# Performance work log

Measured on AMD Instinct MI355X. Metric: run time of the kernel, lower is better.

## Reference

```python
import jax, jax.numpy as jnp
import numpy as np

N, B, L, D = 11, 4, 2048, 1024
EPS = 1e-5


def _layernorm(x, g, b):
    # torch LayerNorm: biased variance over last dim
    mu = x.mean(-1, keepdims=True)
    var = x.var(-1, keepdims=True)
    return (x - mu) / jnp.sqrt(var + EPS) * g + b


def _block_attn_res(V, q, g, b):
    # V: [n, B, L, D] -- completed blocks + current partial
    K = _layernorm(V, g, b)
    logits = jnp.einsum('d,nbld->nbl', q, K)      # single pseudo-query dot
    w = jax.nn.softmax(logits, axis=0)             # softmax over block dim n
    return jnp.einsum('nbl,nbld->bld', w, V)       # weighted sum back to [B,L,D]


def setup_inputs() -> dict:
    key = jax.random.key(0)
    k0, k1, k2 = jax.random.split(key, 3)
    return {
        'streams': jax.random.normal(k0, (N, B, L, D), dtype=jnp.float32),
        'attn_q': jax.random.normal(k1, (N, D), dtype=jnp.float32) * 0.02,
        'attn_gamma': jnp.ones((N, D), dtype=jnp.float32),
        'attn_beta': jnp.zeros((N, D), dtype=jnp.float32),
        'mlp_q': jax.random.normal(k2, (N, D), dtype=jnp.float32) * 0.02,
        'mlp_gamma': jnp.ones((N, D), dtype=jnp.float32),
        'mlp_beta': jnp.zeros((N, D), dtype=jnp.float32),
    }


def reference(streams, attn_q, attn_gamma, attn_beta, mlp_q, mlp_gamma, mlp_beta):
    # streams: [N, B, L, D]; sequential over the small fixed stream count (N=11)
    n = streams.shape[0]
    blocks = []
    updated = []
    for i in range(n):
        partial = streams[i]
        V = jnp.stack(blocks + [partial], axis=0)              # [i+1, B, L, D]
        h = _block_attn_res(V, attn_q[i], attn_gamma[i], attn_beta[i])
        V2 = jnp.stack(blocks + [h], axis=0)
        h = _block_attn_res(V2, mlp_q[i], mlp_gamma[i], mlp_beta[i])
        blocks.append(partial)
        updated.append(h)
    return jnp.stack(updated, axis=0)                          # [N, B, L, D]
```

## Files before the change

kernel.cpp:

```cpp
#include <hip/hip_runtime.h>
#include <math.h>

#define NN 11
#define RR 8192
#define DD 1024
#define EPSV 1e-5f
#define PREP_TPB 256

#define OFF_SCAL 22528
#define OFF_WFRAG 22592

typedef __attribute__((ext_vector_type(8))) short short8;
typedef __attribute__((ext_vector_type(4))) float f32x4;

__device__ __forceinline__ float wave_reduce(float v) {
#pragma unroll
  for (int o = 32; o > 0; o >>= 1) v += __shfl_xor(v, o, 64);
  return v;
}

__device__ __forceinline__ unsigned cvtpk(float lo, float hi) {
  unsigned r;
  asm("v_cvt_pk_bf16_f32 %0, %1, %2" : "=v"(r) : "v"(lo), "v"(hi));
  return r;
}

__device__ __forceinline__ float b2f(unsigned short s) {
  return __uint_as_float(((unsigned)s) << 16);
}

__global__ __launch_bounds__(PREP_TPB) void prep_kernel(
    const float* __restrict__ aq, const float* __restrict__ ag, const float* __restrict__ ab,
    const float* __restrict__ mq, const float* __restrict__ mg, const float* __restrict__ mb,
    float* __restrict__ wvec, float* __restrict__ scal)
{
  const int j = blockIdx.x;
  const float *q, *g, *bt;
  if (j < NN) { q = aq + (size_t)j*DD;      g = ag + (size_t)j*DD;      bt = ab + (size_t)j*DD; }
  else        { q = mq + (size_t)(j-NN)*DD; g = mg + (size_t)(j-NN)*DD; bt = mb + (size_t)(j-NN)*DD; }
  const int t = threadIdx.x;
  float sqg = 0.f, sqb = 0.f;
  for (int d = t; d < DD; d += PREP_TPB) {
    float qq = q[d];
    float w  = qq * g[d];
    wvec[(size_t)j*DD + d] = w;
    sqg += w;
    sqb += qq * bt[d];
  }
  sqg = wave_reduce(sqg);
  sqb = wave_reduce(sqb);
  __shared__ float red[2][PREP_TPB/64];
  const int lane = t & 63, wid = t >> 6;
  if (lane == 0) { red[0][wid] = sqg; red[1][wid] = sqb; }
  __syncthreads();
  if (t == 0) {
    float a = 0.f, b2 = 0.f;
    for (int w = 0; w < PREP_TPB/64; ++w) { a += red[0][w]; b2 += red[1][w]; }
    scal[2*j]   = a;
    scal[2*j+1] = b2;
  }
}

__global__ __launch_bounds__(256) void prep2_kernel(
    const float* __restrict__ wvec, short* __restrict__ wfrag)
{
  const int kstep = blockIdx.x;
  const int t = threadIdx.x;
#pragma unroll
  for (int q = 0; q < 4; ++q) {
    const int idx  = t*4 + q;
    const int c    = idx >> 9;
    const int lane = (idx >> 3) & 63;
    const int e    = idx & 7;
    const int k    = kstep*32 + (lane >> 4)*8 + e;
    const int j    = c*16 + (lane & 15);
    float v = (j < 22) ? wvec[(size_t)j*DD + k] : (j == 22 ? 1.0f : 0.f);
    unsigned u = __float_as_uint(v);
    u = (u + 0x7FFFu + ((u >> 16) & 1u)) >> 16;
    wfrag[(size_t)kstep*1024 + idx] = (short)u;
  }
}

__global__ __launch_bounds__(256) void fused_kernel(
    const float* __restrict__ streams, const short* __restrict__ wfrag,
    const float* __restrict__ scal, float* __restrict__ out)
{
  __shared__ __align__(16) short xt[NN*1024];
  __shared__ float fl4[4*11*40];
  __shared__ float Cs[11][12];

  const int p  = blockIdx.x;
  const int t  = threadIdx.x;
  const int l  = t & 63;
  const int wv = t >> 6;

#pragma unroll
  for (int n = 0; n < NN; ++n) {
    float4 v = *(const float4*)(streams + ((size_t)(n*RR + p))*DD + t*4);
    const int byte = (n*2048 + t*8) ^ ((n & 7) << 4);
    *(uint2*)((char*)xt + byte) = make_uint2(cvtpk(v.x, v.y), cvtpk(v.z, v.w));
  }
  __syncthreads();

  const int lr = l & 15, g = l >> 4;
  const int arow  = (lr < NN) ? lr : (NN-1);
  const int abase = arow*2048;
  const int aswz  = (arow & 7) << 4;

  f32x4 acc0 = {0.f,0.f,0.f,0.f};
  f32x4 acc1 = {0.f,0.f,0.f,0.f};
  f32x4 acc2 = {0.f,0.f,0.f,0.f};
#pragma unroll
  for (int ksl = 0; ksl < 8; ++ksl) {
    const int ks = wv*8 + ksl;
    const int byte = (abase + ks*64 + g*16) ^ aswz;
    short8 af = *(const short8*)((char*)xt + byte);
    const size_t bo = (size_t)ks*1024 + (size_t)l*8;
    short8 b0 = *(const short8*)(wfrag + bo);
    short8 b1 = *(const short8*)(wfrag + bo + 512);
    acc0 = __builtin_amdgcn_mfma_f32_16x16x32_bf16(af, b0, acc0, 0, 0, 0);
    acc1 = __builtin_amdgcn_mfma_f32_16x16x32_bf16(af, b1, acc1, 0, 0, 0);
    acc2 = __builtin_amdgcn_mfma_f32_16x16x32_bf16(af, af, acc2, 0, 0, 0);
  }
  {
    float* R0 = fl4 + wv*440;
#pragma unroll
    for (int r = 0; r < 4; ++r) {
      const int row = g*4 + r;
      if (row < NN) {
        float* R = R0 + row*40;
        R[lr] = acc0[r];
        if (lr <= 6)  R[16 + lr] = acc1[r];
        if (lr < NN)  R[24 + lr] = acc2[r];
      }
    }
  }
  __syncthreads();

  for (int s = t; s < 440; s += 256)
    fl4[s] = fl4[s] + fl4[440 + s] + fl4[880 + s] + fl4[1320 + s];
  __syncthreads();

  if (t < NN) {
    const int i = t;
    const float qgA = scal[2*i],      qbA = scal[2*i+1];
    const float qgM = scal[2*(NN+i)], qbM = scal[2*(NN+i)+1];

    float mu[NN], rs[NN];
#pragma unroll
    for (int n = 0; n < NN; ++n) {
      mu[n] = fl4[n*40 + 22] * (1.f/DD);
      float vr = fl4[n*40 + 24 + n] * (1.f/DD) - mu[n]*mu[n];
      rs[n] = rsqrtf(vr + EPSV);
    }

    float w1[NN], dM[NN];
    float mx = -3.0e38f;
#pragma unroll
    for (int n = 0; n < NN; ++n) {
      w1[n] = 0.f;
      if (n <= i) {
        float lg = (fl4[n*40 + i] - mu[n]*qgA)*rs[n] + qbA;
        w1[n] = lg;
        mx = fmaxf(mx, lg);
      }
    }
    float S = 0.f;
#pragma unroll
    for (int n = 0; n < NN; ++n) if (n <= i) { float e = __expf(w1[n]-mx); w1[n] = e; S += e; }
    const float inv = 1.f/S;
    float muh = 0.f, hd = 0.f;
#pragma unroll
    for (int n = 0; n < NN; ++n) {
      if (n <= i) {
        w1[n] *= inv;
        dM[n] = fl4[n*40 + 11 + i];
        muh += w1[n]*mu[n];
        hd  += w1[n]*dM[n];
      } else w1[n] = 0.f;
    }

    float hss = 0.f;
#pragma unroll
    for (int m = 0; m < NN; ++m) {
      const float wm = w1[m];
      float acc = 0.f;
#pragma unroll
      for (int n = 0; n < NN; ++n) acc = fmaf(w1[n], fl4[m*40 + 24 + n], acc);
      hss = fmaf(wm, acc, hss);
    }
    const float varh = hss*(1.f/DD) - muh*muh;
    const float rsh  = rsqrtf(varh + EPSV);
    const float lgh  = (hd - muh*qgM)*rsh + qbM;

    float lg2[NN], w2[NN];
    float mx2 = lgh;
#pragma unroll
    for (int n = 0; n < NN; ++n) if (n < i) {
      lg2[n] = (dM[n] - mu[n]*qgM)*rs[n] + qbM;
      mx2 = fmaxf(mx2, lg2[n]);
    }
    float eh = __expf(lgh - mx2);
    float S2 = eh;
#pragma unroll
    for (int n = 0; n < NN; ++n) if (n < i) { w2[n] = __expf(lg2[n]-mx2); S2 += w2[n]; }
    const float inv2 = 1.f/S2;
    const float ehw  = eh*inv2;
#pragma unroll
    for (int n = 0; n < NN; ++n) {
      float cc = ehw * w1[n];
      if (n < i) cc += w2[n]*inv2;
      Cs[i][n] = cc;
    }
  }
  __syncthreads();

  const int kt = t*4;
  float xf[NN][4];
#pragma unroll
  for (int n = 0; n < NN; ++n) {
    const int byte = (n*2048 + kt*2) ^ ((n & 7) << 4);
    uint2 u = *(const uint2*)((char*)xt + byte);
    xf[n][0] = b2f((unsigned short)(u.x & 0xFFFF));
    xf[n][1] = b2f((unsigned short)(u.x >> 16));
    xf[n][2] = b2f((unsigned short)(u.y & 0xFFFF));
    xf[n][3] = b2f((unsigned short)(u.y >> 16));
  }
#pragma unroll
  for (int i = 0; i < NN; ++i) {
    float o0 = 0.f, o1 = 0.f, o2 = 0.f, o3 = 0.f;
#pragma unroll
    for (int n = 0; n < NN; ++n) {
      const float c = Cs[i][n];
      o0 = fmaf(c, xf[n][0], o0);
      o1 = fmaf(c, xf[n][1], o1);
      o2 = fmaf(c, xf[n][2], o2);
      o3 = fmaf(c, xf[n][3], o3);
    }
    *(float4*)(out + ((size_t)(i*RR + p))*DD + kt) = make_float4(o0, o1, o2, o3);
  }
}

extern "C" void kernel_launch(void* const* d_in, const int* in_sizes, int n_in,
                              void* d_out, int out_size, void* d_ws, size_t ws_size,
                              hipStream_t stream) {
  const float* streams = (const float*)d_in[0];
  const float* aq = (const float*)d_in[1];
  const float* ag = (const float*)d_in[2];
  const float* ab = (const float*)d_in[3];
  const float* mq = (const float*)d_in[4];
  const float* mg = (const float*)d_in[5];
  const float* mb = (const float*)d_in[6];
  float* outp = (float*)d_out;

  float* wsf   = (float*)d_ws;
  float* wvec  = wsf;
  float* scal  = wsf + OFF_SCAL;
  short* wfrag = (short*)(wsf + OFF_WFRAG);

  prep_kernel<<<dim3(2*NN), dim3(PREP_TPB), 0, stream>>>(aq, ag, ab, mq, mg, mb, wvec, scal);
  prep2_kernel<<<dim3(32), dim3(256), 0, stream>>>(wvec, wfrag);
  fused_kernel<<<dim3(RR), dim3(256), 0, stream>>>(streams, wfrag, scal, outp);
}
```

Baseline: 191.7 us.

## Keep fp32 stream values in registers and give each wave a private LDS slice

Each wave now loads its own 256-column slice of all 11 streams into registers. It converts that slice to bf16 into a wave-private LDS region, so the block-wide barrier before the MFMA stage is no longer needed. The final weighted sum reuses the fp32 register copies instead of re-reading bf16 from LDS, which removes the LDS readback and unpack and uses full-precision values. The cost is 44 extra live fp32 registers per thread across the reduction and softmax stages, which may lower occupancy.

```diff
diff --git a/kernel.cpp b/kernel.cpp
--- a/kernel.cpp
+++ b/kernel.cpp
@@ -23,10 +23,6 @@
   unsigned r;
   asm("v_cvt_pk_bf16_f32 %0, %1, %2" : "=v"(r) : "v"(lo), "v"(hi));
   return r;
-}
-
-__device__ __forceinline__ float b2f(unsigned short s) {
-  return __uint_as_float(((unsigned)s) << 16);
 }
 
 __global__ __launch_bounds__(PREP_TPB) void prep_kernel(
@@ -85,7 +81,7 @@
     const float* __restrict__ streams, const short* __restrict__ wfrag,
     const float* __restrict__ scal, float* __restrict__ out)
 {
-  __shared__ __align__(16) short xt[NN*1024];
+  __shared__ __align__(16) short xt[4*11*256];
   __shared__ float fl4[4*11*40];
   __shared__ float Cs[11][12];
 
@@ -93,18 +89,21 @@
   const int t  = threadIdx.x;
   const int l  = t & 63;
   const int wv = t >> 6;
-
+  const int lr = l & 15, g = l >> 4;
+
+  short* wxt = xt + wv*2816;
+
+  float4 xf[NN];
+#pragma unroll
+  for (int n = 0; n < NN; ++n)
+    xf[n] = *(const float4*)(streams + ((size_t)(n*RR + p))*DD + wv*256 + l*4);
 #pragma unroll
   for (int n = 0; n < NN; ++n) {
-    float4 v = *(const float4*)(streams + ((size_t)(n*RR + p))*DD + t*4);
-    const int byte = (n*2048 + t*8) ^ ((n & 7) << 4);
-    *(uint2*)((char*)xt + byte) = make_uint2(cvtpk(v.x, v.y), cvtpk(v.z, v.w));
-  }
-  __syncthreads();
-
-  const int lr = l & 15, g = l >> 4;
+    const int byte = (n*512 + l*8) ^ ((n & 7) << 4);
+    *(uint2*)((char*)wxt + byte) = make_uint2(cvtpk(xf[n].x, xf[n].y), cvtpk(xf[n].z, xf[n].w));
+  }
+
   const int arow  = (lr < NN) ? lr : (NN-1);
-  const int abase = arow*2048;
   const int aswz  = (arow & 7) << 4;
 
   f32x4 acc0 = {0.f,0.f,0.f,0.f};
@@ -112,10 +111,9 @@
   f32x4 acc2 = {0.f,0.f,0.f,0.f};
 #pragma unroll
   for (int ksl = 0; ksl < 8; ++ksl) {
-    const int ks = wv*8 + ksl;
-    const int byte = (abase + ks*64 + g*16) ^ aswz;
-    short8 af = *(const short8*)((char*)xt + byte);
-    const size_t bo = (size_t)ks*1024 + (size_t)l*8;
+    const int byte = (arow*512 + ksl*64 + g*16) ^ aswz;
+    short8 af = *(const short8*)((char*)wxt + byte);
+    const size_t bo = (size_t)(wv*8 + ksl)*1024 + (size_t)l*8;
     short8 b0 = *(const short8*)(wfrag + bo);
     short8 b1 = *(const short8*)(wfrag + bo + 512);
     acc0 = __builtin_amdgcn_mfma_f32_16x16x32_bf16(af, b0, acc0, 0, 0, 0);
@@ -215,27 +213,17 @@
   }
   __syncthreads();
 
-  const int kt = t*4;
-  float xf[NN][4];
-#pragma unroll
-  for (int n = 0; n < NN; ++n) {
-    const int byte = (n*2048 + kt*2) ^ ((n & 7) << 4);
-    uint2 u = *(const uint2*)((char*)xt + byte);
-    xf[n][0] = b2f((unsigned short)(u.x & 0xFFFF));
-    xf[n][1] = b2f((unsigned short)(u.x >> 16));
-    xf[n][2] = b2f((unsigned short)(u.y & 0xFFFF));
-    xf[n][3] = b2f((unsigned short)(u.y >> 16));
-  }
+  const int kt = wv*256 + l*4;
 #pragma unroll
   for (int i = 0; i < NN; ++i) {
     float o0 = 0.f, o1 = 0.f, o2 = 0.f, o3 = 0.f;
 #pragma unroll
     for (int n = 0; n < NN; ++n) {
       const float c = Cs[i][n];
-      o0 = fmaf(c, xf[n][0], o0);
-      o1 = fmaf(c, xf[n][1], o1);
-      o2 = fmaf(c, xf[n][2], o2);
-      o3 = fmaf(c, xf[n][3], o3);
+      o0 = fmaf(c, xf[n].x, o0);
+      o1 = fmaf(c, xf[n].y, o1);
+      o2 = fmaf(c, xf[n].z, o2);
+      o3 = fmaf(c, xf[n].w, o3);
     }
     *(float4*)(out + ((size_t)(i*RR + p))*DD + kt) = make_float4(o0, o1, o2, o3);
   }
```

Result: slower. 209.7 us (+9.4%).
